# Kernel optimization log

Measured on AMD Instinct MI355X. Metric: run time of the kernel, lower is better.

Reference implementation:

```python
import jax, jax.numpy as jnp
import numpy as np

N_NODES = 100000
N_EDGES = 1600000
IN_FEATS = 128
N_HIDDEN = 64
N_HEADS = 4
N_CLASSES = 16


def setup_inputs() -> dict:
    key = jax.random.key(0)
    ks = jax.random.split(key, 16)
    h = jax.random.normal(ks[0], (N_NODES, IN_FEATS), dtype=jnp.float32)
    src = jax.random.randint(ks[1], (N_EDGES,), 0, N_NODES, dtype=jnp.int32)
    dst = jax.random.randint(ks[2], (N_EDGES,), 0, N_NODES, dtype=jnp.int32)
    def xavier(k, shape, fan_in, fan_out):
        gain = jnp.sqrt(2.0)  # calculate_gain('relu')
        std = gain * jnp.sqrt(2.0 / (fan_in + fan_out))
        return (std * jax.random.normal(k, shape)).astype(jnp.float32)
    # layer 1: per-head W [H, in, out], A [H, 2*out]
    W1 = xavier(ks[3], (N_HEADS, IN_FEATS, N_HIDDEN), IN_FEATS, N_HIDDEN)
    b1 = jnp.zeros((N_HEADS, N_HIDDEN), jnp.float32)
    a1 = xavier(ks[4], (N_HEADS, 2 * N_HIDDEN), 2 * N_HIDDEN, 1)
    ab1 = jnp.zeros((N_HEADS,), jnp.float32)
    # layer 2: input is concat of heads = N_HEADS*N_HIDDEN, output n_classes, heads averaged
    d2 = N_HEADS * N_HIDDEN
    W2 = xavier(ks[5], (N_HEADS, d2, N_CLASSES), d2, N_CLASSES)
    b2 = jnp.zeros((N_HEADS, N_CLASSES), jnp.float32)
    a2 = xavier(ks[6], (N_HEADS, 2 * N_CLASSES), 2 * N_CLASSES, 1)
    ab2 = jnp.zeros((N_HEADS,), jnp.float32)
    fc_w = xavier(ks[7], (N_CLASSES, N_CLASSES), N_CLASSES, N_CLASSES)
    fc_b = jnp.zeros((N_CLASSES,), jnp.float32)
    return dict(h=h, src=src, dst=dst, W1=W1, b1=b1, a1=a1, ab1=ab1,
                W2=W2, b2=b2, a2=a2, ab2=ab2, fc_w=fc_w, fc_b=fc_b)


def gat_layer(h, src, dst, W, b, a, ab, n_nodes):
    # h: [N, F]; W: [H, F, O]; a: [H, 2O]
    O = W.shape[-1]
    Wh = jnp.einsum('nf,hfo->nho', h, W) + b          # [N, H, O]
    Wh_src = Wh[src]                                   # [E, H, O] (messages Wh_j)
    Wh_dst = Wh[dst]                                   # [E, H, O] (Wh_i)
    # e_ij = LeakyReLU(A([Wh_i, Wh_j]), 0.2)
    e = (jnp.einsum('eho,ho->eh', Wh_dst, a[:, :O])
         + jnp.einsum('eho,ho->eh', Wh_src, a[:, O:]) + ab)  # [E, H]
    e = jax.nn.leaky_relu(e, 0.2)
    # segment softmax over incoming edges of each dst node
    m = jax.ops.segment_max(e, dst, num_segments=n_nodes)     # [N, H] (-inf for empty)
    ex = jnp.exp(e - m[dst])
    denom = jax.ops.segment_sum(ex, dst, num_segments=n_nodes)
    alpha = ex / denom[dst]                                    # [E, H]
    # weighted neighbor aggregation (zero for zero-in-degree nodes, as DGL)
    out = jax.ops.segment_sum(alpha[:, :, None] * Wh_src, dst, num_segments=n_nodes)
    return out  # [N, H, O]


def reference(h, src, dst, W1, b1, a1, ab1, W2, b2, a2, ab2, fc_w, fc_b):
    n = h.shape[0]
    # layer 1 (heads concatenated) + ELU; dropout = identity (eval mode)
    h1 = gat_layer(h, src, dst, W1, b1, a1, ab1, n)            # [N, H, n_hidden]
    h1 = jax.nn.elu(h1.reshape(n, -1))                         # [N, H*n_hidden]
    # layer 2 (heads averaged) + softmax over features
    h2 = gat_layer(h1, src, dst, W2, b2, a2, ab2, n).mean(axis=1)  # [N, n_classes]
    h2 = jax.nn.softmax(h2, axis=1)
    # readout: mean over nodes, then fc
    hg = h2.mean(axis=0)                                        # [n_classes]
    return hg @ fc_w.T + fc_b
```

## Files before the change

kernel.cpp:

```cpp
#include <hip/hip_runtime.h>
#include <math.h>

#define N_NODES  100000
#define N_EDGES  1600000
#define IN_F     128
#define HID      64
#define HEADS    4
#define NCLS     16
#define D1       (HEADS*HID)
#define D2       (HEADS*NCLS)

#define SCAN_CHUNK 1024
#define SCAN_NB    ((N_NODES + SCAN_CHUNK - 1) / SCAN_CHUNK)
#define N_NODES_PAD (SCAN_NB * SCAN_CHUNK)
#define RB1 128
#define AGG_BLOCKS 2048
#define AGG_WAVES  (AGG_BLOCKS * 4)

typedef __attribute__((ext_vector_type(8))) short bf16x8_t;
typedef __attribute__((ext_vector_type(4))) float f32x4_t;
typedef __attribute__((ext_vector_type(2))) float f32x2_t;

__device__ __forceinline__ unsigned bf16rne(float x) {
  unsigned u = __float_as_uint(x);
  return (u + 0x7fffu + ((u >> 16) & 1u)) >> 16;
}
__device__ __forceinline__ unsigned packbf2(float lo, float hi) {
  return bf16rne(lo) | (bf16rne(hi) << 16);
}

__global__ __launch_bounds__(256)
void k_zero4(int4* __restrict__ p, int n4) {
  int i = blockIdx.x * blockDim.x + threadIdx.x;
  if (i < n4) p[i] = make_int4(0, 0, 0, 0);
}

__global__ __launch_bounds__(256)
void k_count(const int* __restrict__ dst, int* __restrict__ cursorPad,
             int* __restrict__ rank) {
  int i = blockIdx.x * blockDim.x + threadIdx.x;
  if (i < N_EDGES) {
    int d = dst[i];
    rank[i] = atomicAdd(&cursorPad[d << 4], 1);
  }
}

__global__ __launch_bounds__(256)
void k_compact(const int* __restrict__ cursorPad, int* __restrict__ counts) {
  int i = blockIdx.x * blockDim.x + threadIdx.x;
  if (i < N_NODES_PAD) counts[i] = (i < N_NODES) ? cursorPad[i << 4] : 0;
}

__global__ __launch_bounds__(256)
void k_scanA(const int* __restrict__ counts, int* __restrict__ btot) {
  __shared__ int red[256];
  int t = threadIdx.x;
  const int4* cp = (const int4*)(counts + blockIdx.x * SCAN_CHUNK);
  int4 v = cp[t];
  red[t] = v.x + v.y + v.z + v.w;
  __syncthreads();
  for (int s = 128; s; s >>= 1) {
    if (t < s) red[t] += red[t + s];
    __syncthreads();
  }
  if (t == 0) btot[blockIdx.x] = red[0];
}

__global__ __launch_bounds__(128)
void k_scanB(const int* __restrict__ btot, int* __restrict__ bbase,
             int* __restrict__ offs) {
  __shared__ int part[128];
  int t = threadIdx.x;
  part[t] = (t < SCAN_NB) ? btot[t] : 0;
  __syncthreads();
  for (int o = 1; o < 128; o <<= 1) {
    int v = (t >= o) ? part[t - o] : 0;
    __syncthreads();
    part[t] += v;
    __syncthreads();
  }
  if (t < SCAN_NB) bbase[t] = (t == 0) ? 0 : part[t - 1];
  if (t == 0) offs[N_NODES] = N_EDGES;
}

__global__ __launch_bounds__(256)
void k_scanC(const int* __restrict__ counts, const int* __restrict__ bbase,
             int* __restrict__ offs) {
  __shared__ int part[256];
  int t = threadIdx.x;
  int gbase = blockIdx.x * SCAN_CHUNK;
  const int4* cp = (const int4*)(counts + gbase);
  int4 v = cp[t];
  int tot = v.x + v.y + v.z + v.w;
  part[t] = tot;
  __syncthreads();
  for (int o = 1; o < 256; o <<= 1) {
    int q = (t >= o) ? part[t - o] : 0;
    __syncthreads();
    part[t] += q;
    __syncthreads();
  }
  int run = bbase[blockIdx.x] + part[t] - tot;
  int i0 = gbase + t * 4;
  int o0 = run;
  int o1 = o0 + v.x;
  int o2 = o1 + v.y;
  int o3 = o2 + v.z;
  if (i0 + 0 < N_NODES) offs[i0 + 0] = o0;
  if (i0 + 1 < N_NODES) offs[i0 + 1] = o1;
  if (i0 + 2 < N_NODES) offs[i0 + 2] = o2;
  if (i0 + 3 < N_NODES) offs[i0 + 3] = o3;
}

__global__ __launch_bounds__(256)
void k_scatter(const int* __restrict__ src, const int* __restrict__ dst,
               const int* __restrict__ rank, const int* __restrict__ offs,
               int* __restrict__ csrsrc) {
  int i = blockIdx.x * blockDim.x + threadIdx.x;
  if (i < N_EDGES) {
    csrsrc[offs[dst[i]] + rank[i]] = src[i];
  }
}

__global__ __launch_bounds__(256)
void k_prepw(const float* __restrict__ W1, const float* __restrict__ W2,
             unsigned* __restrict__ W1t32, unsigned* __restrict__ W2t32) {
  int t = threadIdx.x;
  if (blockIdx.x == 0) {
    int c = t;
    const float* wp = W1 + ((c >> 6) << 13) + (c & 63);
    unsigned* op = W1t32 + c * 64;
    for (int fp = 0; fp < 64; ++fp) {
      float lo = wp[(2 * fp) << 6];
      float hi = wp[(2 * fp + 1) << 6];
      op[fp] = packbf2(lo, hi);
    }
  } else {
    int c = t & 63, fq = t >> 6;
    const float* wp = W2 + ((c >> 4) << 12) + (c & 15);
    unsigned* op = W2t32 + c * 128 + fq * 32;
    for (int fp = 0; fp < 32; ++fp) {
      int f0 = fq * 64 + 2 * fp;
      op[fp] = packbf2(wp[f0 << 4], wp[(f0 + 1) << 4]);
    }
  }
}

__global__ __launch_bounds__(256)
void k_gemm1(const float* __restrict__ h, const unsigned short* __restrict__ W1t,
             const float* __restrict__ bias, const float* __restrict__ a1,
             unsigned char* __restrict__ Wh8,
             float* __restrict__ sD, float* __restrict__ sS) {
  __shared__ float aLds[512];
  int t = threadIdx.x;
  aLds[t] = a1[t];
  aLds[t + 256] = a1[t + 256];
  __syncthreads();

  int wv = t >> 6;
  int lane = t & 63;
  int m = lane & 15;
  int q8 = (lane >> 4) * 8;
  int node = blockIdx.x * 64 + wv * 16 + m;
  int nclamp = node < N_NODES ? node : N_NODES - 1;

  f32x4_t acc[16] = {};
  const float* hp0 = h + (size_t)nclamp * IN_F + q8;
  #pragma unroll
  for (int ks = 0; ks < 4; ++ks) {
    int kk = ks * 32;
    float4 f0 = *(const float4*)(hp0 + kk);
    float4 f1 = *(const float4*)(hp0 + kk + 4);
    bf16x8_t bf;
    bf[0] = (short)bf16rne(f0.x); bf[1] = (short)bf16rne(f0.y);
    bf[2] = (short)bf16rne(f0.z); bf[3] = (short)bf16rne(f0.w);
    bf[4] = (short)bf16rne(f1.x); bf[5] = (short)bf16rne(f1.y);
    bf[6] = (short)bf16rne(f1.z); bf[7] = (short)bf16rne(f1.w);
    #pragma unroll
    for (int ct = 0; ct < 16; ++ct) {
      bf16x8_t af = *(const bf16x8_t*)(W1t + (ct * 16 + m) * IN_F + kk + q8);
      acc[ct] = __builtin_amdgcn_mfma_f32_16x16x32_bf16(af, bf, acc[ct], 0, 0, 0);
    }
  }
  if (node < N_NODES) {
    unsigned char* op = Wh8 + (size_t)node * D1;
    int quad4 = (lane >> 4) * 4;
    float pd[4] = {}, ps[4] = {};
    #pragma unroll
    for (int ct = 0; ct < 16; ++ct) {
      int c0 = ct * 16 + quad4;
      float4 bb = *(const float4*)(bias + c0);
      float v0 = acc[ct][0] + bb.x, v1 = acc[ct][1] + bb.y;
      float v2 = acc[ct][2] + bb.z, v3 = acc[ct][3] + bb.w;
      int hh = ct >> 2;
      const float* aD = &aLds[hh * 128 + (c0 & 63)];
      pd[hh] += v0 * aD[0] + v1 * aD[1] + v2 * aD[2] + v3 * aD[3];
      ps[hh] += v0 * aD[64] + v1 * aD[65] + v2 * aD[66] + v3 * aD[67];
      int pk = __builtin_amdgcn_cvt_pk_fp8_f32(v0, v1, 0, false);
      pk = __builtin_amdgcn_cvt_pk_fp8_f32(v2, v3, pk, true);
      *(unsigned*)(op + c0) = (unsigned)pk;
    }
    #pragma unroll
    for (int hh = 0; hh < 4; ++hh) {
      pd[hh] += __shfl_xor(pd[hh], 16); pd[hh] += __shfl_xor(pd[hh], 32);
      ps[hh] += __shfl_xor(ps[hh], 16); ps[hh] += __shfl_xor(ps[hh], 32);
    }
    if (lane < 16) {
      ((float4*)sD)[node] = make_float4(pd[0], pd[1], pd[2], pd[3]);
      ((float4*)sS)[node] = make_float4(ps[0], ps[1], ps[2], ps[3]);
    }
  }
}

__global__ __launch_bounds__(256)
void k_gemm2(const unsigned short* __restrict__ h1b, const unsigned short* __restrict__ W2t,
             const float* __restrict__ bias, const float* __restrict__ a2,
             unsigned short* __restrict__ Whb2,
             float* __restrict__ sD, float* __restrict__ sS) {
  __shared__ float aLds[128];
  int t = threadIdx.x;
  if (t < 128) aLds[t] = a2[t];
  __syncthreads();

  int wv = t >> 6;
  int lane = t & 63;
  int m = lane & 15;
  int q8 = (lane >> 4) * 8;
  int node = blockIdx.x * 64 + wv * 16 + m;
  int nclamp = node < N_NODES ? node : N_NODES - 1;

  f32x4_t acc[4] = {};
  const unsigned short* hp0 = h1b + (size_t)nclamp * D1 + q8;
  #pragma unroll
  for (int ks = 0; ks < 8; ++ks) {
    int kk = ks * 32;
    bf16x8_t bf = *(const bf16x8_t*)(hp0 + kk);
    #pragma unroll
    for (int ct = 0; ct < 4; ++ct) {
      bf16x8_t af = *(const bf16x8_t*)(W2t + (ct * 16 + m) * D1 + kk + q8);
      acc[ct] = __builtin_amdgcn_mfma_f32_16x16x32_bf16(af, bf, acc[ct], 0, 0, 0);
    }
  }
  if (node < N_NODES) {
    unsigned short* op = Whb2 + (size_t)node * D2;
    int quad4 = (lane >> 4) * 4;
    float pd[4] = {}, ps[4] = {};
    #pragma unroll
    for (int ct = 0; ct < 4; ++ct) {
      int c0 = ct * 16 + quad4;
      float4 bb = *(const float4*)(bias + c0);
      float v0 = acc[ct][0] + bb.x, v1 = acc[ct][1] + bb.y;
      float v2 = acc[ct][2] + bb.z, v3 = acc[ct][3] + bb.w;
      const float* aD = &aLds[ct * 32 + (c0 & 15)];
      pd[ct] += v0 * aD[0] + v1 * aD[1] + v2 * aD[2] + v3 * aD[3];
      ps[ct] += v0 * aD[16] + v1 * aD[17] + v2 * aD[18] + v3 * aD[19];
      uint2 o;
      o.x = packbf2(v0, v1);
      o.y = packbf2(v2, v3);
      *(uint2*)(op + c0) = o;
    }
    #pragma unroll
    for (int hh = 0; hh < 4; ++hh) {
      pd[hh] += __shfl_xor(pd[hh], 16); pd[hh] += __shfl_xor(pd[hh], 32);
      ps[hh] += __shfl_xor(ps[hh], 16); ps[hh] += __shfl_xor(ps[hh], 32);
    }
    if (lane < 16) {
      ((float4*)sD)[node] = make_float4(pd[0], pd[1], pd[2], pd[3]);
      ((float4*)sS)[node] = make_float4(ps[0], ps[1], ps[2], ps[3]);
    }
  }
}

__device__ __forceinline__ float lrelu(float x) { return x > 0.f ? x : 0.2f * x; }
__device__ __forceinline__ float elu(float x)   { return x > 0.f ? x : expm1f(x); }

__global__ __launch_bounds__(256)
void k_agg1(const int* __restrict__ offs, const int* __restrict__ csrsrc,
            const float* __restrict__ sD, const float* __restrict__ sS,
            const float* __restrict__ ab,
            const unsigned char* __restrict__ Wh8, unsigned short* __restrict__ h1out) {
  __shared__ float exbuf[4][64 * 4];
  __shared__ int   offbuf[4][64];
  int wv = threadIdx.x >> 6;
  int lane = threadIdx.x & 63;
  int g = lane >> 5;
  int l = lane & 31;
  int hh = l >> 3;
  unsigned lb = (unsigned)(l << 3);
  float ab0 = ab[0], ab1 = ab[1], ab2 = ab[2], ab3 = ab[3];
  const float* eb = exbuf[wv];
  const int* ob = offbuf[wv];

  for (int wid = blockIdx.x * 4 + wv; wid < N_NODES; wid += AGG_WAVES) {
    float acc[8] = {};
    float z0 = 0.f, z1 = 0.f, z2 = 0.f, z3 = 0.f;
    int beg = offs[wid], end = offs[wid + 1];
    bool nonempty = end > beg;
    if (nonempty) {
      float4 dv = ((const float4*)sD)[wid];
      float db0 = dv.x + ab0, db1 = dv.y + ab1;
      float db2 = dv.z + ab2, db3 = dv.w + ab3;
      for (int cbeg = beg; cbeg < end; cbeg += 64) {
        int j = cbeg + lane;
        int cnt = end - cbeg; if (cnt > 64) cnt = 64;
        int sid = 0;
        float e0 = 0.f, e1 = 0.f, e2 = 0.f, e3 = 0.f;
        if (j < end) {
          sid = csrsrc[j];
          float4 sv = ((const float4*)sS)[sid];
          e0 = __expf(lrelu(db0 + sv.x));
          e1 = __expf(lrelu(db1 + sv.y));
          e2 = __expf(lrelu(db2 + sv.z));
          e3 = __expf(lrelu(db3 + sv.w));
          z0 += e0; z1 += e1; z2 += e2; z3 += e3;
        }
        offbuf[wv][lane] = sid << 8;
        *(float4*)&exbuf[wv][lane * 4] = make_float4(e0, e1, e2, e3);
        int npairs = (cnt + 1) >> 1;
        for (int u = 0; u < npairs; ++u) {
          int i0 = 2 * u + g;
          float w = eb[i0 * 4 + hh];
          unsigned voff = (unsigned)ob[i0] + lb;
          uint2 p = *(const uint2*)(Wh8 + voff);
          f32x2_t d0 = __builtin_amdgcn_cvt_pk_f32_fp8(p.x, false);
          f32x2_t d1 = __builtin_amdgcn_cvt_pk_f32_fp8(p.x, true);
          f32x2_t d2 = __builtin_amdgcn_cvt_pk_f32_fp8(p.y, false);
          f32x2_t d3 = __builtin_amdgcn_cvt_pk_f32_fp8(p.y, true);
          acc[0] = fmaf(w, d0[0], acc[0]);
          acc[1] = fmaf(w, d0[1], acc[1]);
          acc[2] = fmaf(w, d1[0], acc[2]);
          acc[3] = fmaf(w, d1[1], acc[3]);
          acc[4] = fmaf(w, d2[0], acc[4]);
          acc[5] = fmaf(w, d2[1], acc[5]);
          acc[6] = fmaf(w, d3[0], acc[6]);
          acc[7] = fmaf(w, d3[1], acc[7]);
        }
      }
      #pragma unroll
      for (int o = 32; o; o >>= 1) {
        z0 += __shfl_xor(z0, o);
        z1 += __shfl_xor(z1, o);
        z2 += __shfl_xor(z2, o);
        z3 += __shfl_xor(z3, o);
      }
    }
    #pragma unroll
    for (int i = 0; i < 8; ++i) acc[i] += __shfl_xor(acc[i], 32);
    float z = (hh == 0) ? z0 : (hh == 1) ? z1 : (hh == 2) ? z2 : z3;
    if (!nonempty) z = 1.f;
    float inv = 1.f / z;
    if (g == 0) {
      float e0 = elu(acc[0] * inv), e1 = elu(acc[1] * inv);
      float e2 = elu(acc[2] * inv), e3 = elu(acc[3] * inv);
      float e4 = elu(acc[4] * inv), e5 = elu(acc[5] * inv);
      float e6 = elu(acc[6] * inv), e7 = elu(acc[7] * inv);
      uint4 o;
      o.x = packbf2(e0, e1);
      o.y = packbf2(e2, e3);
      o.z = packbf2(e4, e5);
      o.w = packbf2(e6, e7);
      *(uint4*)(h1out + (size_t)wid * D1 + l * 8) = o;
    }
  }
}

__global__ __launch_bounds__(256)
void k_agg2(const int* __restrict__ offs, const int* __restrict__ csrsrc,
            const float* __restrict__ sD, const float* __restrict__ sS,
            const float* __restrict__ ab,
            const unsigned short* __restrict__ Whb2, float* __restrict__ partials) {
  __shared__ float exbuf[4][64 * 4];
  __shared__ int   offbuf[4][64];
  __shared__ float red[4][16];
  int wv = threadIdx.x >> 6;
  int lane = threadIdx.x & 63;
  int g = lane >> 4;
  int l = lane & 15;
  int hh = l >> 2;
  unsigned lb = (unsigned)(l << 3);
  float ab0 = ab[0], ab1 = ab[1], ab2 = ab[2], ab3 = ab[3];
  const float* eb = exbuf[wv];
  const int* ob = offbuf[wv];
  float smacc[4] = {};

  for (int wid = blockIdx.x * 4 + wv; wid < N_NODES; wid += AGG_WAVES) {
    float acc[4] = {};
    float z0 = 0.f, z1 = 0.f, z2 = 0.f, z3 = 0.f;
    int beg = offs[wid], end = offs[wid + 1];
    bool nonempty = end > beg;
    if (nonempty) {
      float4 dv = ((const float4*)sD)[wid];
      float db0 = dv.x + ab0, db1 = dv.y + ab1;
      float db2 = dv.z + ab2, db3 = dv.w + ab3;
      for (int cbeg = beg; cbeg < end; cbeg += 64) {
        int j = cbeg + lane;
        int cnt = end - cbeg; if (cnt > 64) cnt = 64;
        if (j < end) {
          int sid = csrsrc[j];
          float4 sv = ((const float4*)sS)[sid];
          float e0 = __expf(lrelu(db0 + sv.x));
          float e1 = __expf(lrelu(db1 + sv.y));
          float e2 = __expf(lrelu(db2 + sv.z));
          float e3 = __expf(lrelu(db3 + sv.w));
          z0 += e0; z1 += e1; z2 += e2; z3 += e3;
          offbuf[wv][lane] = sid << 7;
          *(float4*)&exbuf[wv][lane * 4] = make_float4(e0, e1, e2, e3);
        }
        int iters = (cnt + 3) >> 2;
        for (int it = 0; it < iters; ++it) {
          int qq = 4 * it + g;
          int idx = qq < cnt ? qq : cnt - 1;
          float w = eb[idx * 4 + hh];
          if (qq >= cnt) w = 0.f;
          unsigned voff = (unsigned)ob[idx] + lb;
          uint2 p = *(const uint2*)((const unsigned char*)Whb2 + voff);
          acc[0] = fmaf(w, __uint_as_float(p.x << 16), acc[0]);
          acc[1] = fmaf(w, __uint_as_float(p.x), acc[1]);
          acc[2] = fmaf(w, __uint_as_float(p.y << 16), acc[2]);
          acc[3] = fmaf(w, __uint_as_float(p.y), acc[3]);
        }
      }
      #pragma unroll
      for (int s = 32; s; s >>= 1) {
        z0 += __shfl_xor(z0, s);
        z1 += __shfl_xor(z1, s);
        z2 += __shfl_xor(z2, s);
        z3 += __shfl_xor(z3, s);
      }
    }
    #pragma unroll
    for (int i = 0; i < 4; ++i) {
      acc[i] += __shfl_xor(acc[i], 16);
      acc[i] += __shfl_xor(acc[i], 32);
    }
    float z = (hh == 0) ? z0 : (hh == 1) ? z1 : (hh == 2) ? z2 : z3;
    if (!nonempty) z = 1.f;
    float inv = 1.f / z;
    float val[4];
    #pragma unroll
    for (int i = 0; i < 4; ++i) val[i] = acc[i] * inv;
    #pragma unroll
    for (int i = 0; i < 4; ++i) {
      val[i] += __shfl_xor(val[i], 4);
      val[i] += __shfl_xor(val[i], 8);
      val[i] *= 0.25f;
    }
    float mx = fmaxf(fmaxf(val[0], val[1]), fmaxf(val[2], val[3]));
    mx = fmaxf(mx, __shfl_xor(mx, 1));
    mx = fmaxf(mx, __shfl_xor(mx, 2));
    float e[4];
    float ssum = 0.f;
    #pragma unroll
    for (int i = 0; i < 4; ++i) { e[i] = __expf(val[i] - mx); ssum += e[i]; }
    ssum += __shfl_xor(ssum, 1);
    ssum += __shfl_xor(ssum, 2);
    float rinv = 1.f / ssum;
    #pragma unroll
    for (int i = 0; i < 4; ++i) smacc[i] += e[i] * rinv;
  }

  if (g == 0 && l < 4) {
    #pragma unroll
    for (int i = 0; i < 4; ++i) red[wv][l * 4 + i] = smacc[i];
  }
  __syncthreads();
  if (threadIdx.x < 16) {
    partials[(size_t)blockIdx.x * 16 + threadIdx.x] =
        red[0][threadIdx.x] + red[1][threadIdx.x] +
        red[2][threadIdx.x] + red[3][threadIdx.x];
  }
}

__global__ __launch_bounds__(256)
void k_reduce1(const float* __restrict__ partials, int nrows,
               float* __restrict__ out) {
  __shared__ float red[16][17];
  int t = threadIdx.x;
  int c = t & 15, rl = t >> 4;
  int per = (nrows + RB1 - 1) / RB1;
  int rbeg = blockIdx.x * per;
  int rend = rbeg + per; if (rend > nrows) rend = nrows;
  float s = 0.f;
  for (int r = rbeg + rl; r < rend; r += 16) s += partials[(size_t)r * 16 + c];
  red[rl][c] = s;
  __syncthreads();
  for (int st = 8; st; st >>= 1) {
    if (rl < st) red[rl][c] += red[rl + st][c];
    __syncthreads();
  }
  if (t < 16) out[(size_t)blockIdx.x * 16 + t] = red[0][t];
}

__global__ __launch_bounds__(256)
void k_final(const float* __restrict__ partials,
             const float* __restrict__ fcw, const float* __restrict__ fcb,
             float* __restrict__ out) {
  __shared__ float red[16][17];
  __shared__ float hg[16];
  int t = threadIdx.x;
  int c = t & 15, rl = t >> 4;
  float s = 0.f;
  for (int r = rl; r < RB1; r += 16) s += partials[(size_t)r * 16 + c];
  red[rl][c] = s;
  __syncthreads();
  for (int st = 8; st; st >>= 1) {
    if (rl < st) red[rl][c] += red[rl + st][c];
    __syncthreads();
  }
  if (t < 16) hg[t] = red[0][t] * (1.0f / N_NODES);
  __syncthreads();
  if (t < 16) {
    float acc = fcb[t];
    #pragma unroll
    for (int k = 0; k < 16; ++k) acc += hg[k] * fcw[t * 16 + k];
    out[t] = acc;
  }
}

extern "C" void kernel_launch(void* const* d_in, const int* in_sizes, int n_in,
                              void* d_out, int out_size, void* d_ws, size_t ws_size,
                              hipStream_t stream) {
  const float* h   = (const float*)d_in[0];
  const int*   src = (const int*)  d_in[1];
  const int*   dst = (const int*)  d_in[2];
  const float* W1  = (const float*)d_in[3];
  const float* b1  = (const float*)d_in[4];
  const float* a1  = (const float*)d_in[5];
  const float* ab1 = (const float*)d_in[6];
  const float* W2  = (const float*)d_in[7];
  const float* b2  = (const float*)d_in[8];
  const float* a2  = (const float*)d_in[9];
  const float* ab2 = (const float*)d_in[10];
  const float* fcw = (const float*)d_in[11];
  const float* fcb = (const float*)d_in[12];
  float* out = (float*)d_out;

  char* ws = (char*)d_ws;
  size_t off = 0;
  auto alloc = [&](size_t bytes) -> char* {
    char* p = ws + off;
    off += (bytes + 255) & ~(size_t)255;
    return p;
  };
  unsigned char*  Wh8  = (unsigned char*)alloc((size_t)N_NODES * D1);
  unsigned short* h1b  = (unsigned short*)alloc((size_t)N_NODES * D1 * 2);
  unsigned short* Whb2 = (unsigned short*)alloc((size_t)N_NODES * D2 * 2);
  unsigned short* W1t  = (unsigned short*)alloc((size_t)D1 * IN_F * 2);
  unsigned short* W2t  = (unsigned short*)alloc((size_t)D2 * D1 * 2);
  float* sD1 = (float*)alloc((size_t)N_NODES * 4 * 4);
  float* sS1 = (float*)alloc((size_t)N_NODES * 4 * 4);
  float* sD2 = (float*)alloc((size_t)N_NODES * 4 * 4);
  float* sS2 = (float*)alloc((size_t)N_NODES * 4 * 4);
  int* cursorPad = (int*)alloc((size_t)N_NODES * 16 * 4);
  int* rank   = (int*)alloc((size_t)N_EDGES * 4);
  int* counts = (int*)alloc((size_t)N_NODES_PAD * 4);
  int* offs   = (int*)alloc((size_t)(N_NODES + 1) * 4);
  int* csrsrc = (int*)alloc((size_t)N_EDGES * 4);
  int* btot   = (int*)alloc((size_t)SCAN_NB * 4);
  int* bbase  = (int*)alloc((size_t)SCAN_NB * 4);
  float* partials  = (float*)alloc((size_t)AGG_BLOCKS * 16 * 4);
  float* partials2 = (float*)alloc((size_t)RB1 * 16 * 4);

  k_prepw<<<2, 256, 0, stream>>>(W1, W2, (unsigned*)W1t, (unsigned*)W2t);

  const int n4 = N_NODES * 4;
  k_zero4<<<(n4 + 255) / 256, 256, 0, stream>>>((int4*)cursorPad, n4);
  k_count<<<(N_EDGES + 255) / 256, 256, 0, stream>>>(dst, cursorPad, rank);
  k_compact<<<(N_NODES_PAD + 255) / 256, 256, 0, stream>>>(cursorPad, counts);
  k_scanA<<<SCAN_NB, 256, 0, stream>>>(counts, btot);
  k_scanB<<<1, 128, 0, stream>>>(btot, bbase, offs);
  k_scanC<<<SCAN_NB, 256, 0, stream>>>(counts, bbase, offs);
  k_scatter<<<(N_EDGES + 255) / 256, 256, 0, stream>>>(src, dst, rank, offs, csrsrc);

  const int gemmBlocks = (N_NODES + 63) / 64;

  k_gemm1<<<gemmBlocks, 256, 0, stream>>>(h, W1t, b1, a1, Wh8, sD1, sS1);
  k_agg1<<<AGG_BLOCKS, 256, 0, stream>>>(offs, csrsrc, sD1, sS1, ab1, Wh8, h1b);

  k_gemm2<<<gemmBlocks, 256, 0, stream>>>(h1b, W2t, b2, a2, Whb2, sD2, sS2);
  k_agg2<<<AGG_BLOCKS, 256, 0, stream>>>(offs, csrsrc, sD2, sS2, ab2, Whb2, partials);

  k_reduce1<<<RB1, 256, 0, stream>>>(partials, AGG_BLOCKS, partials2);
  k_final<<<1, 256, 0, stream>>>(partials2, fcw, fcb, out);
}
```

Baseline: 482.3 us.

## Fuse setup kernels and unroll aggregation gathers with packed FMA

Zeroing the cursor array is merged into the weight-prep kernel, and the edge-count atomics are merged into the layer-1 GEMM launch as extra blocks, so they run alongside the GEMM and fewer launches are needed. Both aggregation kernels now store the row offset and edge weight together in one interleaved LDS buffer. Their inner loops are unrolled four ways to issue four independent gathers at once, with accumulation done through packed two-wide FMAs. Lanes past the edge count write zero weights, so the unrolled loop can run over padded slots without masking, at the cost of some wasted gathers of row 0 and more register pressure.

```diff
diff --git a/kernel.cpp b/kernel.cpp
--- a/kernel.cpp
+++ b/kernel.cpp
@@ -16,6 +16,9 @@
 #define RB1 128
 #define AGG_BLOCKS 2048
 #define AGG_WAVES  (AGG_BLOCKS * 4)
+#define GEMM1_BLOCKS ((N_NODES + 63) / 64)
+#define CNT_BLOCKS   ((N_EDGES + 255) / 256)
+#define ZERO_BLOCKS  ((N_NODES * 4 + 255) / 256)
 
 typedef __attribute__((ext_vector_type(8))) short bf16x8_t;
 typedef __attribute__((ext_vector_type(4))) float f32x4_t;
@@ -28,20 +31,35 @@
 __device__ __forceinline__ unsigned packbf2(float lo, float hi) {
   return bf16rne(lo) | (bf16rne(hi) << 16);
 }
-
-__global__ __launch_bounds__(256)
-void k_zero4(int4* __restrict__ p, int n4) {
-  int i = blockIdx.x * blockDim.x + threadIdx.x;
-  if (i < n4) p[i] = make_int4(0, 0, 0, 0);
-}
-
-__global__ __launch_bounds__(256)
-void k_count(const int* __restrict__ dst, int* __restrict__ cursorPad,
-             int* __restrict__ rank) {
-  int i = blockIdx.x * blockDim.x + threadIdx.x;
-  if (i < N_EDGES) {
-    int d = dst[i];
-    rank[i] = atomicAdd(&cursorPad[d << 4], 1);
+__device__ __forceinline__ f32x2_t pkfma(f32x2_t a, f32x2_t b, f32x2_t c) {
+  return __builtin_elementwise_fma(a, b, c);
+}
+
+__global__ __launch_bounds__(256)
+void k_prep(const float* __restrict__ W1, const float* __restrict__ W2,
+            unsigned* __restrict__ W1t32, unsigned* __restrict__ W2t32,
+            int4* __restrict__ cursorPad4) {
+  int t = threadIdx.x;
+  if (blockIdx.x == 0) {
+    int c = t;
+    const float* wp = W1 + ((c >> 6) << 13) + (c & 63);
+    unsigned* op = W1t32 + c * 64;
+    for (int fp = 0; fp < 64; ++fp) {
+      float lo = wp[(2 * fp) << 6];
+      float hi = wp[(2 * fp + 1) << 6];
+      op[fp] = packbf2(lo, hi);
+    }
+  } else if (blockIdx.x == 1) {
+    int c = t & 63, fq = t >> 6;
+    const float* wp = W2 + ((c >> 4) << 12) + (c & 15);
+    unsigned* op = W2t32 + c * 128 + fq * 32;
+    for (int fp = 0; fp < 32; ++fp) {
+      int f0 = fq * 64 + 2 * fp;
+      op[fp] = packbf2(wp[f0 << 4], wp[(f0 + 1) << 4]);
+    }
+  } else {
+    int i = (blockIdx.x - 2) * 256 + t;
+    if (i < N_NODES * 4) cursorPad4[i] = make_int4(0, 0, 0, 0);
   }
 }
 
@@ -123,36 +141,22 @@
 }
 
 __global__ __launch_bounds__(256)
-void k_prepw(const float* __restrict__ W1, const float* __restrict__ W2,
-             unsigned* __restrict__ W1t32, unsigned* __restrict__ W2t32) {
-  int t = threadIdx.x;
-  if (blockIdx.x == 0) {
-    int c = t;
-    const float* wp = W1 + ((c >> 6) << 13) + (c & 63);
-    unsigned* op = W1t32 + c * 64;
-    for (int fp = 0; fp < 64; ++fp) {
-      float lo = wp[(2 * fp) << 6];
-      float hi = wp[(2 * fp + 1) << 6];
-      op[fp] = packbf2(lo, hi);
-    }
-  } else {
-    int c = t & 63, fq = t >> 6;
-    const float* wp = W2 + ((c >> 4) << 12) + (c & 15);
-    unsigned* op = W2t32 + c * 128 + fq * 32;
-    for (int fp = 0; fp < 32; ++fp) {
-      int f0 = fq * 64 + 2 * fp;
-      op[fp] = packbf2(wp[f0 << 4], wp[(f0 + 1) << 4]);
-    }
-  }
-}
-
-__global__ __launch_bounds__(256)
-void k_gemm1(const float* __restrict__ h, const unsigned short* __restrict__ W1t,
-             const float* __restrict__ bias, const float* __restrict__ a1,
-             unsigned char* __restrict__ Wh8,
-             float* __restrict__ sD, float* __restrict__ sS) {
+void k_gemm1cnt(const float* __restrict__ h, const unsigned short* __restrict__ W1t,
+                const float* __restrict__ bias, const float* __restrict__ a1,
+                unsigned char* __restrict__ Wh8,
+                float* __restrict__ sD, float* __restrict__ sS,
+                const int* __restrict__ dst, int* __restrict__ cursorPad,
+                int* __restrict__ rank) {
   __shared__ float aLds[512];
   int t = threadIdx.x;
+  if (blockIdx.x >= GEMM1_BLOCKS) {
+    int i = (blockIdx.x - GEMM1_BLOCKS) * 256 + t;
+    if (i < N_EDGES) {
+      int d = dst[i];
+      rank[i] = atomicAdd(&cursorPad[d << 4], 1);
+    }
+    return;
+  }
   aLds[t] = a1[t];
   aLds[t + 256] = a1[t + 256];
   __syncthreads();
@@ -279,8 +283,7 @@
             const float* __restrict__ sD, const float* __restrict__ sS,
             const float* __restrict__ ab,
             const unsigned char* __restrict__ Wh8, unsigned short* __restrict__ h1out) {
-  __shared__ float exbuf[4][64 * 4];
-  __shared__ int   offbuf[4][64];
+  __shared__ uint2 ewbuf[4][64 * 4];
   int wv = threadIdx.x >> 6;
   int lane = threadIdx.x & 63;
   int g = lane >> 5;
@@ -288,11 +291,10 @@
   int hh = l >> 3;
   unsigned lb = (unsigned)(l << 3);
   float ab0 = ab[0], ab1 = ab[1], ab2 = ab[2], ab3 = ab[3];
-  const float* eb = exbuf[wv];
-  const int* ob = offbuf[wv];
+  const uint2* eb = ewbuf[wv];
 
   for (int wid = blockIdx.x * 4 + wv; wid < N_NODES; wid += AGG_WAVES) {
-    float acc[8] = {};
+    f32x2_t acc[4] = {};
     float z0 = 0.f, z1 = 0.f, z2 = 0.f, z3 = 0.f;
     int beg = offs[wid], end = offs[wid + 1];
     bool nonempty = end > beg;
@@ -314,26 +316,55 @@
           e3 = __expf(lrelu(db3 + sv.w));
           z0 += e0; z1 += e1; z2 += e2; z3 += e3;
         }
-        offbuf[wv][lane] = sid << 8;
-        *(float4*)&exbuf[wv][lane * 4] = make_float4(e0, e1, e2, e3);
+        unsigned ro = (unsigned)(sid << 8);
+        uint2* wp = &ewbuf[wv][lane * 4];
+        wp[0] = make_uint2(ro, __float_as_uint(e0));
+        wp[1] = make_uint2(ro, __float_as_uint(e1));
+        wp[2] = make_uint2(ro, __float_as_uint(e2));
+        wp[3] = make_uint2(ro, __float_as_uint(e3));
         int npairs = (cnt + 1) >> 1;
-        for (int u = 0; u < npairs; ++u) {
+        int nh = (npairs + 3) >> 2;
+        for (int u = 0; u < nh; ++u) {
           int i0 = 2 * u + g;
-          float w = eb[i0 * 4 + hh];
-          unsigned voff = (unsigned)ob[i0] + lb;
-          uint2 p = *(const uint2*)(Wh8 + voff);
-          f32x2_t d0 = __builtin_amdgcn_cvt_pk_f32_fp8(p.x, false);
-          f32x2_t d1 = __builtin_amdgcn_cvt_pk_f32_fp8(p.x, true);
-          f32x2_t d2 = __builtin_amdgcn_cvt_pk_f32_fp8(p.y, false);
-          f32x2_t d3 = __builtin_amdgcn_cvt_pk_f32_fp8(p.y, true);
-          acc[0] = fmaf(w, d0[0], acc[0]);
-          acc[1] = fmaf(w, d0[1], acc[1]);
-          acc[2] = fmaf(w, d1[0], acc[2]);
-          acc[3] = fmaf(w, d1[1], acc[3]);
-          acc[4] = fmaf(w, d2[0], acc[4]);
-          acc[5] = fmaf(w, d2[1], acc[5]);
-          acc[6] = fmaf(w, d3[0], acc[6]);
-          acc[7] = fmaf(w, d3[1], acc[7]);
+          int i1 = i0 + 2 * nh;
+          int i2 = i0 + 4 * nh;
+          int i3 = i0 + 6 * nh;
+          uint2 ew0 = eb[i0 * 4 + hh];
+          uint2 ew1 = eb[i1 * 4 + hh];
+          uint2 ew2 = eb[i2 * 4 + hh];
+          uint2 ew3 = eb[i3 * 4 + hh];
+          uint2 p0 = *(const uint2*)(Wh8 + (ew0.x + lb));
+          uint2 p1 = *(const uint2*)(Wh8 + (ew1.x + lb));
+          uint2 p2 = *(const uint2*)(Wh8 + (ew2.x + lb));
+          uint2 p3 = *(const uint2*)(Wh8 + (ew3.x + lb));
+          {
+            float w = __uint_as_float(ew0.y); f32x2_t w2 = {w, w};
+            acc[0] = pkfma(w2, __builtin_amdgcn_cvt_pk_f32_fp8(p0.x, false), acc[0]);
+            acc[1] = pkfma(w2, __builtin_amdgcn_cvt_pk_f32_fp8(p0.x, true ), acc[1]);
+            acc[2] = pkfma(w2, __builtin_amdgcn_cvt_pk_f32_fp8(p0.y, false), acc[2]);
+            acc[3] = pkfma(w2, __builtin_amdgcn_cvt_pk_f32_fp8(p0.y, true ), acc[3]);
+          }
+          {
+            float w = __uint_as_float(ew1.y); f32x2_t w2 = {w, w};
+            acc[0] = pkfma(w2, __builtin_amdgcn_cvt_pk_f32_fp8(p1.x, false), acc[0]);
+            acc[1] = pkfma(w2, __builtin_amdgcn_cvt_pk_f32_fp8(p1.x, true ), acc[1]);
+            acc[2] = pkfma(w2, __builtin_amdgcn_cvt_pk_f32_fp8(p1.y, false), acc[2]);
+            acc[3] = pkfma(w2, __builtin_amdgcn_cvt_pk_f32_fp8(p1.y, true ), acc[3]);
+          }
+          {
+            float w = __uint_as_float(ew2.y); f32x2_t w2 = {w, w};
+            acc[0] = pkfma(w2, __builtin_amdgcn_cvt_pk_f32_fp8(p2.x, false), acc[0]);
+            acc[1] = pkfma(w2, __builtin_amdgcn_cvt_pk_f32_fp8(p2.x, true ), acc[1]);
+            acc[2] = pkfma(w2, __builtin_amdgcn_cvt_pk_f32_fp8(p2.y, false), acc[2]);
+            acc[3] = pkfma(w2, __builtin_amdgcn_cvt_pk_f32_fp8(p2.y, true ), acc[3]);
+          }
+          {
+            float w = __uint_as_float(ew3.y); f32x2_t w2 = {w, w};
+            acc[0] = pkfma(w2, __builtin_amdgcn_cvt_pk_f32_fp8(p3.x, false), acc[0]);
+            acc[1] = pkfma(w2, __builtin_amdgcn_cvt_pk_f32_fp8(p3.x, true ), acc[1]);
+            acc[2] = pkfma(w2, __builtin_amdgcn_cvt_pk_f32_fp8(p3.y, false), acc[2]);
+            acc[3] = pkfma(w2, __builtin_amdgcn_cvt_pk_f32_fp8(p3.y, true ), acc[3]);
+          }
         }
       }
       #pragma unroll
@@ -345,20 +376,19 @@
       }
     }
     #pragma unroll
-    for (int i = 0; i < 8; ++i) acc[i] += __shfl_xor(acc[i], 32);
+    for (int i = 0; i < 4; ++i) {
+      acc[i][0] += __shfl_xor(acc[i][0], 32);
+      acc[i][1] += __shfl_xor(acc[i][1], 32);
+    }
     float z = (hh == 0) ? z0 : (hh == 1) ? z1 : (hh == 2) ? z2 : z3;
     if (!nonempty) z = 1.f;
     float inv = 1.f / z;
     if (g == 0) {
-      float e0 = elu(acc[0] * inv), e1 = elu(acc[1] * inv);
-      float e2 = elu(acc[2] * inv), e3 = elu(acc[3] * inv);
-      float e4 = elu(acc[4] * inv), e5 = elu(acc[5] * inv);
-      float e6 = elu(acc[6] * inv), e7 = elu(acc[7] * inv);
       uint4 o;
-      o.x = packbf2(e0, e1);
-      o.y = packbf2(e2, e3);
-      o.z = packbf2(e4, e5);
-      o.w = packbf2(e6, e7);
+      o.x = packbf2(elu(acc[0][0] * inv), elu(acc[0][1] * inv));
+      o.y = packbf2(elu(acc[1][0] * inv), elu(acc[1][1] * inv));
+      o.z = packbf2(elu(acc[2][0] * inv), elu(acc[2][1] * inv));
+      o.w = packbf2(elu(acc[3][0] * inv), elu(acc[3][1] * inv));
       *(uint4*)(h1out + (size_t)wid * D1 + l * 8) = o;
     }
   }
@@ -369,8 +399,7 @@
             const float* __restrict__ sD, const float* __restrict__ sS,
             const float* __restrict__ ab,
             const unsigned short* __restrict__ Whb2, float* __restrict__ partials) {
-  __shared__ float exbuf[4][64 * 4];
-  __shared__ int   offbuf[4][64];
+  __shared__ uint2 ewbuf[4][64 * 4];
   __shared__ float red[4][16];
   int wv = threadIdx.x >> 6;
   int lane = threadIdx.x & 63;
@@ -379,12 +408,11 @@
   int hh = l >> 2;
   unsigned lb = (unsigned)(l << 3);
   float ab0 = ab[0], ab1 = ab[1], ab2 = ab[2], ab3 = ab[3];
-  const float* eb = exbuf[wv];
-  const int* ob = offbuf[wv];
+  const uint2* eb = ewbuf[wv];
   float smacc[4] = {};
 
   for (int wid = blockIdx.x * 4 + wv; wid < N_NODES; wid += AGG_WAVES) {
-    float acc[4] = {};
+    f32x2_t acc[2] = {};
     float z0 = 0.f, z1 = 0.f, z2 = 0.f, z3 = 0.f;
     int beg = offs[wid], end = offs[wid + 1];
     bool nonempty = end > beg;
@@ -395,29 +423,71 @@
       for (int cbeg = beg; cbeg < end; cbeg += 64) {
         int j = cbeg + lane;
         int cnt = end - cbeg; if (cnt > 64) cnt = 64;
+        int sid = 0;
+        float e0 = 0.f, e1 = 0.f, e2 = 0.f, e3 = 0.f;
         if (j < end) {
-          int sid = csrsrc[j];
+          sid = csrsrc[j];
           float4 sv = ((const float4*)sS)[sid];
-          float e0 = __expf(lrelu(db0 + sv.x));
-          float e1 = __expf(lrelu(db1 + sv.y));
-          float e2 = __expf(lrelu(db2 + sv.z));
-          float e3 = __expf(lrelu(db3 + sv.w));
+          e0 = __expf(lrelu(db0 + sv.x));
+          e1 = __expf(lrelu(db1 + sv.y));
+          e2 = __expf(lrelu(db2 + sv.z));
+          e3 = __expf(lrelu(db3 + sv.w));
           z0 += e0; z1 += e1; z2 += e2; z3 += e3;
-          offbuf[wv][lane] = sid << 7;
-          *(float4*)&exbuf[wv][lane * 4] = make_float4(e0, e1, e2, e3);
         }
-        int iters = (cnt + 3) >> 2;
-        for (int it = 0; it < iters; ++it) {
-          int qq = 4 * it + g;
-          int idx = qq < cnt ? qq : cnt - 1;
-          float w = eb[idx * 4 + hh];
-          if (qq >= cnt) w = 0.f;
-          unsigned voff = (unsigned)ob[idx] + lb;
-          uint2 p = *(const uint2*)((const unsigned char*)Whb2 + voff);
-          acc[0] = fmaf(w, __uint_as_float(p.x << 16), acc[0]);
-          acc[1] = fmaf(w, __uint_as_float(p.x), acc[1]);
-          acc[2] = fmaf(w, __uint_as_float(p.y << 16), acc[2]);
-          acc[3] = fmaf(w, __uint_as_float(p.y), acc[3]);
+        unsigned ro = (unsigned)(sid << 7);
+        uint2* wp = &ewbuf[wv][lane * 4];
+        wp[0] = make_uint2(ro, __float_as_uint(e0));
+        wp[1] = make_uint2(ro, __float_as_uint(e1));
+        wp[2] = make_uint2(ro, __float_as_uint(e2));
+        wp[3] = make_uint2(ro, __float_as_uint(e3));
+        int ni = (cnt + 3) >> 2;
+        int nq = (ni + 3) >> 2;
+        for (int u = 0; u < nq; ++u) {
+          int q0 = 4 * u + g;
+          int q1 = q0 + 4 * nq;
+          int q2 = q0 + 8 * nq;
+          int q3 = q0 + 12 * nq;
+          uint2 ew0 = eb[q0 * 4 + hh];
+          uint2 ew1 = eb[q1 * 4 + hh];
+          uint2 ew2 = eb[q2 * 4 + hh];
+          uint2 ew3 = eb[q3 * 4 + hh];
+          const unsigned char* base = (const unsigned char*)Whb2;
+          uint2 p0 = *(const uint2*)(base + (ew0.x + lb));
+          uint2 p1 = *(const uint2*)(base + (ew1.x + lb));
+          uint2 p2 = *(const uint2*)(base + (ew2.x + lb));
+          uint2 p3 = *(const uint2*)(base + (ew3.x + lb));
+          {
+            float w = __uint_as_float(ew0.y); f32x2_t w2 = {w, w};
+            f32x2_t dA, dB;
+            dA[0] = __uint_as_float(p0.x << 16); dA[1] = __uint_as_float(p0.x & 0xffff0000u);
+            dB[0] = __uint_as_float(p0.y << 16); dB[1] = __uint_as_float(p0.y & 0xffff0000u);
+            acc[0] = pkfma(w2, dA, acc[0]);
+            acc[1] = pkfma(w2, dB, acc[1]);
+          }
+          {
+            float w = __uint_as_float(ew1.y); f32x2_t w2 = {w, w};
+            f32x2_t dA, dB;
+            dA[0] = __uint_as_float(p1.x << 16); dA[1] = __uint_as_float(p1.x & 0xffff0000u);
+            dB[0] = __uint_as_float(p1.y << 16); dB[1] = __uint_as_float(p1.y & 0xffff0000u);
+            acc[0] = pkfma(w2, dA, acc[0]);
+            acc[1] = pkfma(w2, dB, acc[1]);
+          }
+          {
+            float w = __uint_as_float(ew2.y); f32x2_t w2 = {w, w};
+            f32x2_t dA, dB;
+            dA[0] = __uint_as_float(p2.x << 16); dA[1] = __uint_as_float(p2.x & 0xffff0000u);
+            dB[0] = __uint_as_float(p2.y << 16); dB[1] = __uint_as_float(p2.y & 0xffff0000u);
+            acc[0] = pkfma(w2, dA, acc[0]);
+            acc[1] = pkfma(w2, dB, acc[1]);
+          }
+          {
+            float w = __uint_as_float(ew3.y); f32x2_t w2 = {w, w};
+            f32x2_t dA, dB;
+            dA[0] = __uint_as_float(p3.x << 16); dA[1] = __uint_as_float(p3.x & 0xffff0000u);
+            dB[0] = __uint_as_float(p3.y << 16); dB[1] = __uint_as_float(p3.y & 0xffff0000u);
+            acc[0] = pkfma(w2, dA, acc[0]);
+            acc[1] = pkfma(w2, dB, acc[1]);
+          }
         }
       }
       #pragma unroll
@@ -429,16 +499,20 @@
       }
     }
     #pragma unroll
-    for (int i = 0; i < 4; ++i) {
-      acc[i] += __shfl_xor(acc[i], 16);
-      acc[i] += __shfl_xor(acc[i], 32);
+    for (int i = 0; i < 2; ++i) {
+      acc[i][0] += __shfl_xor(acc[i][0], 16);
+      acc[i][1] += __shfl_xor(acc[i][1], 16);
+      acc[i][0] += __shfl_xor(acc[i][0], 32);
+      acc[i][1] += __shfl_xor(acc[i][1], 32);
     }
     float z = (hh == 0) ? z0 : (hh == 1) ? z1 : (hh == 2) ? z2 : z3;
     if (!nonempty) z = 1.f;
     float inv = 1.f / z;
     float val[4];
-    #pragma unroll
-    for (int i = 0; i < 4; ++i) val[i] = acc[i] * inv;
+    val[0] = acc[0][0] * inv;
+    val[1] = acc[0][1] * inv;
+    val[2] = acc[1][0] * inv;
+    val[3] = acc[1][1] * inv;
     #pragma unroll
     for (int i = 0; i < 4; ++i) {
       val[i] += __shfl_xor(val[i], 4);
@@ -561,23 +635,21 @@
   float* partials  = (float*)alloc((size_t)AGG_BLOCKS * 16 * 4);
   float* partials2 = (float*)alloc((size_t)RB1 * 16 * 4);
 
-  k_prepw<<<2, 256, 0, stream>>>(W1, W2, (unsigned*)W1t, (unsigned*)W2t);
-
-  const int n4 = N_NODES * 4;
-  k_zero4<<<(n4 + 255) / 256, 256, 0, stream>>>((int4*)cursorPad, n4);
-  k_count<<<(N_EDGES + 255) / 256, 256, 0, stream>>>(dst, cursorPad, rank);
+  k_prep<<<2 + ZERO_BLOCKS, 256, 0, stream>>>(W1, W2, (unsigned*)W1t, (unsigned*)W2t,
+                                              (int4*)cursorPad);
+
+  k_gemm1cnt<<<GEMM1_BLOCKS + CNT_BLOCKS, 256, 0, stream>>>(
+      h, W1t, b1, a1, Wh8, sD1, sS1, dst, cursorPad, rank);
+
   k_compact<<<(N_NODES_PAD + 255) / 256, 256, 0, stream>>>(cursorPad, counts);
   k_scanA<<<SCAN_NB, 256, 0, stream>>>(counts, btot);
   k_scanB<<<1, 128, 0, stream>>>(btot, bbase, offs);
   k_scanC<<<SCAN_NB, 256, 0, stream>>>(counts, bbase, offs);
-  k_scatter<<<(N_EDGES + 255) / 256, 256, 0, stream>>>(src, dst, rank, offs, csrsrc);
-
-  const int gemmBlocks = (N_NODES + 63) / 64;
-
-  k_gemm1<<<gemmBlocks, 256, 0, stream>>>(h, W1t, b1, a1, Wh8, sD1, sS1);
+  k_scatter<<<CNT_BLOCKS, 256, 0, stream>>>(src, dst, rank, offs, csrsrc);
+
   k_agg1<<<AGG_BLOCKS, 256, 0, stream>>>(offs, csrsrc, sD1, sS1, ab1, Wh8, h1b);
 
-  k_gemm2<<<gemmBlocks, 256, 0, stream>>>(h1b, W2t, b2, a2, Whb2, sD2, sS2);
+  k_gemm2<<<GEMM1_BLOCKS, 256, 0, stream>>>(h1b, W2t, b2, a2, Whb2, sD2, sS2);
   k_agg2<<<AGG_BLOCKS, 256, 0, stream>>>(offs, csrsrc, sD2, sS2, ab2, Whb2, partials);
 
   k_reduce1<<<RB1, 256, 0, stream>>>(partials, AGG_BLOCKS, partials2);
```

After: 478.1 us. Within noise of the previous version (-0.9%).
